# Performance work log

Hardware: AMD Instinct MI355X
Metric: run time of the kernel (lower is better)

## Reference

```python
import jax, jax.numpy as jnp
import numpy as np

X_CH, Y_CH, DIM, NUM_HEAD = 256, 512, 128, 4
H_DIM = DIM // NUM_HEAD
GAMMA = H_DIM ** (-0.5)


def conv1x1(x, w, b):
    # x: [B,C,H,W], w: [O,C], b: [O]
    return jnp.einsum('bchw,oc->bohw', x, w) + b[None, :, None, None]


def _split_qkv(qkv, bs, hw):
    # qkv: [B, 3*DIM, H, W] -> q,k,v each [B, NUM_HEAD, HW, H_DIM]
    qkv = qkv.reshape(bs, 3, NUM_HEAD, H_DIM, hw)
    qkv = jnp.transpose(qkv, (1, 0, 2, 4, 3))  # [3, B, H, HW, D]
    return qkv[0], qkv[1], qkv[2]


def setup_inputs() -> dict:
    key = jax.random.key(0)
    ks = jax.random.split(key, 12)
    s = lambda fan_in: 1.0 / np.sqrt(fan_in)
    x = jax.random.normal(ks[0], (2, X_CH, 64, 64), dtype=jnp.float32)
    y = jax.random.normal(ks[1], (2, Y_CH, 32, 32), dtype=jnp.float32)
    wx_qkv = jax.random.normal(ks[2], (3 * DIM, X_CH), dtype=jnp.float32) * s(X_CH)
    bx_qkv = jax.random.normal(ks[3], (3 * DIM,), dtype=jnp.float32) * s(X_CH)
    wy_qkv = jax.random.normal(ks[4], (3 * DIM, Y_CH), dtype=jnp.float32) * s(Y_CH)
    by_qkv = jax.random.normal(ks[5], (3 * DIM,), dtype=jnp.float32) * s(Y_CH)
    wpx = jax.random.normal(ks[6], (X_CH, DIM), dtype=jnp.float32) * s(DIM)
    bpx = jax.random.normal(ks[7], (X_CH,), dtype=jnp.float32) * s(DIM)
    wpy = jax.random.normal(ks[8], (Y_CH, DIM), dtype=jnp.float32) * s(DIM)
    bpy = jax.random.normal(ks[9], (Y_CH,), dtype=jnp.float32) * s(DIM)
    return {"x": x, "y": y, "wx_qkv": wx_qkv, "bx_qkv": bx_qkv,
            "wy_qkv": wy_qkv, "by_qkv": by_qkv,
            "wpx": wpx, "bpx": bpx, "wpy": wpy, "bpy": bpy}


def reference(x, y, wx_qkv, bx_qkv, wy_qkv, by_qkv, wpx, bpx, wpy, bpy):
    bs, _, h_x, w_x = x.shape
    _, _, h_y, w_y = y.shape
    hw_x, hw_y = h_x * w_x, h_y * w_y

    q_x, k_x, v_x = _split_qkv(conv1x1(x, wx_qkv, bx_qkv), bs, hw_x)
    q_y, k_y, v_y = _split_qkv(conv1x1(y, wy_qkv, by_qkv), bs, hw_y)

    # x attends to y
    atten_x = jax.nn.softmax(jnp.einsum('bhqd,bhkd->bhqk', q_x, k_y) * GAMMA, axis=-1)
    out_x = jnp.einsum('bhqk,bhkd->bhqd', atten_x, v_y)  # [B,H,HWx,D]
    out_x = jnp.transpose(out_x, (0, 1, 3, 2)).reshape(bs, DIM, h_x, w_x)

    # y attends to x
    atten_y = jax.nn.softmax(jnp.einsum('bhqd,bhkd->bhqk', q_y, k_x) * GAMMA, axis=-1)
    out_y = jnp.einsum('bhqk,bhkd->bhqd', atten_y, v_x)
    out_y = jnp.transpose(out_y, (0, 1, 3, 2)).reshape(bs, DIM, h_y, w_y)

    out_x = conv1x1(out_x, wpx, bpx) + x
    out_y = conv1x1(out_y, wpy, bpy) + y
    return out_x, out_y
```

## Files before the change

kernel.cpp:

```cpp
#include <hip/hip_runtime.h>
#include <hip/hip_bf16.h>
#include <cstdint>

#define B 2
#define NH 4
#define HD 32
#define DIM 128
#define CX 256
#define CY 512
#define PX 4096
#define PY 1024
#define QKV 384
#define GAMMA 0.17677669529663687f

typedef unsigned short u16;
typedef unsigned int u32;

using short8 = __attribute__((ext_vector_type(8))) short;
using f32x4  = __attribute__((ext_vector_type(4))) float;

__device__ __forceinline__ float bf2f(u32 h) {
  union { u32 u; float f; } v; v.u = (h & 0xffffu) << 16; return v.f;
}
__device__ __forceinline__ u16 f2bf(float f) {
  u32 u = __float_as_uint(f);
  u32 r = (u + 0x7fffu + ((u >> 16) & 1u)) >> 16;
  return (u16)r;
}
__device__ __forceinline__ bool is_f32(const void* src) {
  u32 u = ((const u16*)src)[2 * (threadIdx.x & 63)];
  return __ballot((u & 0x7F80u) >= 0x4600u) != 0ull;
}

#define N_X   (B * CX * PX)
#define N_Y   (B * CY * PY)
#define N_WX  (QKV * CX)
#define N_BX  (QKV)
#define N_WY  (QKV * CY)
#define N_BY  (QKV)
#define N_WPX (CX * DIM)
#define N_BPX (CX)
#define N_WPY (CY * DIM)
#define N_BPY (CY)

enum : size_t {
  OFF_CWX   = 0,
  OFF_CBX   = OFF_CWX  + N_WX,
  OFF_CWY   = OFF_CBX  + N_BX,
  OFF_CBY   = OFF_CWY  + N_WY,
  OFF_CWPX  = OFF_CBY  + N_BY,
  OFF_CBPX  = OFF_CWPX + N_WPX,
  OFF_CWPY  = OFF_CBPX + N_BPX,
  OFF_CBPY  = OFF_CWPY + N_WPY,
  OFF_XT    = OFF_CBPY + N_BPY,
  OFF_YT    = OFF_XT   + (size_t)B * PX * CX,
  OFF_QPX   = OFF_YT   + (size_t)B * PY * CY,
  OFF_KPX   = OFF_QPX  + (size_t)B * NH * PX * HD,
  OFF_QPY   = OFF_KPX  + (size_t)B * NH * PX * HD,
  OFF_KPY   = OFF_QPY  + (size_t)B * NH * PY * HD,
  OFF_VCX   = OFF_KPY  + (size_t)B * NH * PY * HD,
  OFF_VCY   = OFF_VCX  + (size_t)B * DIM * PX,
  OFF_OTX   = OFF_VCY  + (size_t)B * DIM * PY,
  OFF_OTY   = OFF_OTX  + (size_t)B * PX * DIM,
  WS_END    = OFF_OTY  + (size_t)B * PY * DIM,
};

#define XPX_BLKS 2048
#define XPY_BLKS 1024
__global__ __launch_bounds__(256) void k_prep(
    const void* x, const void* y, const void* wx, const void* bx,
    const void* wy, const void* by, const void* wpx, const void* bpx,
    const void* wpy, const void* bpy, u16* __restrict__ ws) {
  const int id = blockIdx.x;
  if (id < XPX_BLKS + XPY_BLKS) {
    __shared__ u16 tile[32][33];
    const void* src; u16* dst; int C, P, p_t, c_t, b;
    if (id < XPX_BLKS) {
      src = x; dst = ws + OFF_XT; C = CX; P = PX;
      p_t = id & 127; c_t = (id >> 7) & 7; b = id >> 10;
    } else {
      int id2 = id - XPX_BLKS;
      src = y; dst = ws + OFF_YT; C = CY; P = PY;
      p_t = id2 & 31; c_t = (id2 >> 5) & 15; b = id2 >> 9;
    }
    const bool f32in = is_f32(src);
    const int tx = threadIdx.x & 31, ty = threadIdx.x >> 5;
    const int p0 = p_t * 32, c0 = c_t * 32;
#pragma unroll
    for (int i = 0; i < 4; i++) {
      int cl = ty * 4 + i;
      size_t sidx = ((size_t)b * C + c0 + cl) * P + p0 + tx;
      u16 v = f32in ? f2bf(((const float*)src)[sidx]) : ((const u16*)src)[sidx];
      tile[cl][tx] = v;
    }
    __syncthreads();
#pragma unroll
    for (int i = 0; i < 4; i++) {
      int pl = ty * 4 + i;
      dst[((size_t)b * P + p0 + pl) * C + c0 + tx] = tile[tx][pl];
    }
  } else {
    int wid = id - (XPX_BLKS + XPY_BLKS);
    const void* src; size_t dstoff; int n, base;
    if      (wid < 48)  { src = wx;  dstoff = OFF_CWX;  n = N_WX;  base = 0; }
    else if (wid < 49)  { src = bx;  dstoff = OFF_CBX;  n = N_BX;  base = 48; }
    else if (wid < 145) { src = wy;  dstoff = OFF_CWY;  n = N_WY;  base = 49; }
    else if (wid < 146) { src = by;  dstoff = OFF_CBY;  n = N_BY;  base = 145; }
    else if (wid < 162) { src = wpx; dstoff = OFF_CWPX; n = N_WPX; base = 146; }
    else if (wid < 163) { src = bpx; dstoff = OFF_CBPX; n = N_BPX; base = 162; }
    else if (wid < 195) { src = wpy; dstoff = OFF_CWPY; n = N_WPY; base = 163; }
    else                { src = bpy; dstoff = OFF_CBPY; n = N_BPY; base = 195; }
    const bool f32in = is_f32(src);
    int e0 = (wid - base) * 2048 + threadIdx.x * 8;
    if (e0 >= n) return;
    u16* dst = ws + dstoff + e0;
    if (f32in) {
      const float* s = (const float*)src + e0;
      float4 a = *(const float4*)s;
      float4 bq = *(const float4*)(s + 4);
      ushort4 o0, o1;
      o0.x = f2bf(a.x);  o0.y = f2bf(a.y);  o0.z = f2bf(a.z);  o0.w = f2bf(a.w);
      o1.x = f2bf(bq.x); o1.y = f2bf(bq.y); o1.z = f2bf(bq.z); o1.w = f2bf(bq.w);
      *(ushort4*)dst = o0;
      *(ushort4*)(dst + 4) = o1;
    } else {
      uint4 v = *(const uint4*)((const u16*)src + e0);
      *(uint4*)dst = v;
    }
  }
}

__global__ __launch_bounds__(256) void k_qkv(u16* __restrict__ ws) {
  const int t = threadIdx.x;
  const int lane = t & 63, w = t >> 6;
  const int ql = lane & 15, quad = lane >> 4;
  const int b = blockIdx.z;

  const u16 *W, *Xt, *bias; u16 *qp, *kp, *vc; int C, P, pxb;
  if (blockIdx.x < 64) {
    W = ws + OFF_CWX; Xt = ws + OFF_XT; bias = ws + OFF_CBX;
    qp = ws + OFF_QPX; kp = ws + OFF_KPX; vc = ws + OFF_VCX;
    C = CX; P = PX; pxb = blockIdx.x;
  } else {
    W = ws + OFF_CWY; Xt = ws + OFF_YT; bias = ws + OFF_CBY;
    qp = ws + OFF_QPY; kp = ws + OFF_KPY; vc = ws + OFF_VCY;
    C = CY; P = PY; pxb = blockIdx.x - 64;
  }
  const int p_w = pxb * 64 + (w & 1) * 32;
  const int o_w = blockIdx.y * 64 + (w >> 1) * 32;

  const u16* wr0 = W + (size_t)(o_w + ql) * C;
  const u16* wr1 = W + (size_t)(o_w + 16 + ql) * C;
  const u16* xr0 = Xt + ((size_t)b * P + p_w + ql) * C;
  const u16* xr1 = Xt + ((size_t)b * P + p_w + 16 + ql) * C;

  union U { uint4 u; short8 s; };
  f32x4 acc[2][2];
#pragma unroll
  for (int i = 0; i < 2; i++)
#pragma unroll
    for (int j = 0; j < 2; j++) acc[i][j] = (f32x4){0.f, 0.f, 0.f, 0.f};

#pragma unroll 4
  for (int c0 = 0; c0 < C; c0 += 32) {
    int off = c0 + quad * 8;
    U a0, a1, b0, b1;
    a0.u = *(const uint4*)&wr0[off];
    a1.u = *(const uint4*)&wr1[off];
    b0.u = *(const uint4*)&xr0[off];
    b1.u = *(const uint4*)&xr1[off];
    acc[0][0] = __builtin_amdgcn_mfma_f32_16x16x32_bf16(a0.s, b0.s, acc[0][0], 0, 0, 0);
    acc[0][1] = __builtin_amdgcn_mfma_f32_16x16x32_bf16(a0.s, b1.s, acc[0][1], 0, 0, 0);
    acc[1][0] = __builtin_amdgcn_mfma_f32_16x16x32_bf16(a1.s, b0.s, acc[1][0], 0, 0, 0);
    acc[1][1] = __builtin_amdgcn_mfma_f32_16x16x32_bf16(a1.s, b1.s, acc[1][1], 0, 0, 0);
  }

  float bs[2][4];
#pragma unroll
  for (int oi = 0; oi < 2; oi++)
#pragma unroll
    for (int r = 0; r < 4; r++)
      bs[oi][r] = bf2f(bias[o_w + oi * 16 + quad * 4 + r]);

  if (blockIdx.y < 4) {
    bool isq = blockIdx.y < 2;
    float scale = isq ? GAMMA : 1.0f;
    u16* dstT = isq ? qp : kp;
#pragma unroll
    for (int oi = 0; oi < 2; oi++)
#pragma unroll
      for (int pi = 0; pi < 2; pi++) {
        int p = p_w + pi * 16 + ql;
        int o = o_w + oi * 16 + quad * 4 - (isq ? 0 : 128);
        int hh = o >> 5, d = o & 31;
        f32x4 a = acc[oi][pi];
        uint2 pk;
        pk.x = (u32)f2bf((a[0] + bs[oi][0]) * scale) |
               ((u32)f2bf((a[1] + bs[oi][1]) * scale) << 16);
        pk.y = (u32)f2bf((a[2] + bs[oi][2]) * scale) |
               ((u32)f2bf((a[3] + bs[oi][3]) * scale) << 16);
        *(uint2*)&dstT[((size_t)(b * NH + hh) * P + p) * HD + d] = pk;
      }
  } else {
#pragma unroll
    for (int oi = 0; oi < 2; oi++)
#pragma unroll
      for (int pi = 0; pi < 2; pi++) {
        int p = p_w + pi * 16 + ql;
        f32x4 a = acc[oi][pi];
#pragma unroll
        for (int r = 0; r < 4; r++) {
          int o = o_w + oi * 16 + quad * 4 + r - 256;
          vc[((size_t)b * DIM + o) * P + p] = f2bf(a[r] + bs[oi][r]);
        }
      }
  }
}

template <int NQF>
__device__ __forceinline__ void attn_core(
    const u16* __restrict__ Qp, const u16* __restrict__ Kp,
    const u16* __restrict__ Vc, u16* __restrict__ Ot, int Pq, int Pk,
    int q0, int h, int b, u16* pool, float (*mlb)[4][64]) {
  const int t = threadIdx.x;
  const int lane = t & 63, w = t >> 6;
  const int ql = lane & 15, quad = lane >> 4;

  union U { uint4 u; short8 s; };
  U qf[NQF];
#pragma unroll
  for (int qi = 0; qi < NQF; qi++)
    qf[qi].u = *(const uint4*)&Qp[((size_t)(b * NH + h) * Pq + q0 + qi * 16 + ql) * HD + quad * 8];

  const int kspan = Pk >> 2;
  const int kk0 = w * kspan;
  const int niter = kspan >> 5;
  const int f0 = ((ql >> 2) << 3) | (ql & 3);

  const u16* kbase = Kp + ((size_t)(b * NH + h) * Pk + kk0 + f0) * HD + quad * 8;
  const u16* v0base = Vc + ((size_t)(b * DIM + h * HD + ql)) * Pk + kk0 + quad * 8;
  const u16* v1base = v0base + (size_t)16 * Pk;

  U ka, kb, va, vb, kan, kbn, van, vbn;
  ka.u = *(const uint4*)&kbase[0];
  kb.u = *(const uint4*)&kbase[4 * HD];
  va.u = *(const uint4*)&v0base[0];
  vb.u = *(const uint4*)&v1base[0];

  f32x4 o0[NQF], o1[NQF];
  float m_run[NQF], l_run[NQF];
#pragma unroll
  for (int qi = 0; qi < NQF; qi++) {
    o0[qi] = (f32x4){0.f, 0.f, 0.f, 0.f};
    o1[qi] = (f32x4){0.f, 0.f, 0.f, 0.f};
    m_run[qi] = -1e30f; l_run[qi] = 0.f;
  }

  for (int it = 0; it < niter; it++) {
    if (it + 1 < niter) {
      size_t go = (size_t)(it + 1) * 32;
      kan.u = *(const uint4*)&kbase[go * HD];
      kbn.u = *(const uint4*)&kbase[(go + 4) * HD];
      van.u = *(const uint4*)&v0base[go];
      vbn.u = *(const uint4*)&v1base[go];
    }

#pragma unroll
    for (int qi = 0; qi < NQF; qi++) {
      f32x4 z = {0.f, 0.f, 0.f, 0.f};
      f32x4 st0 = __builtin_amdgcn_mfma_f32_16x16x32_bf16(ka.s, qf[qi].s, z, 0, 0, 0);
      f32x4 st1 = __builtin_amdgcn_mfma_f32_16x16x32_bf16(kb.s, qf[qi].s, z, 0, 0, 0);

      float s[8] = {st0[0], st0[1], st0[2], st0[3], st1[0], st1[1], st1[2], st1[3]};
      float cm = fmaxf(fmaxf(fmaxf(s[0], s[1]), fmaxf(s[2], s[3])),
                       fmaxf(fmaxf(s[4], s[5]), fmaxf(s[6], s[7])));
      cm = fmaxf(cm, __shfl_xor(cm, 16));
      cm = fmaxf(cm, __shfl_xor(cm, 32));
      float m_new = fmaxf(m_run[qi], cm);
      float alpha = __expf(m_run[qi] - m_new);
      float p[8], ls = 0.f;
#pragma unroll
      for (int i = 0; i < 8; i++) { p[i] = __expf(s[i] - m_new); ls += p[i]; }
      ls += __shfl_xor(ls, 16);
      ls += __shfl_xor(ls, 32);
      l_run[qi] = l_run[qi] * alpha + ls;
      m_run[qi] = m_new;
#pragma unroll
      for (int r = 0; r < 4; r++) { o0[qi][r] *= alpha; o1[qi][r] *= alpha; }

      U pf;
      pf.u.x = __builtin_amdgcn_perm(__float_as_uint(p[1]), __float_as_uint(p[0]), 0x07060302u);
      pf.u.y = __builtin_amdgcn_perm(__float_as_uint(p[3]), __float_as_uint(p[2]), 0x07060302u);
      pf.u.z = __builtin_amdgcn_perm(__float_as_uint(p[5]), __float_as_uint(p[4]), 0x07060302u);
      pf.u.w = __builtin_amdgcn_perm(__float_as_uint(p[7]), __float_as_uint(p[6]), 0x07060302u);

      o0[qi] = __builtin_amdgcn_mfma_f32_16x16x32_bf16(va.s, pf.s, o0[qi], 0, 0, 0);
      o1[qi] = __builtin_amdgcn_mfma_f32_16x16x32_bf16(vb.s, pf.s, o1[qi], 0, 0, 0);
    }
    ka = kan; kb = kbn; va = van; vb = vbn;
  }

  float* Of = (float*)(pool + (size_t)w * 4096);
#pragma unroll
  for (int qi = 0; qi < NQF; qi++) {
#pragma unroll
    for (int r = 0; r < 4; r++) {
      Of[(qi * 16 + ql) * 32 + quad * 4 + r] = o0[qi][r];
      Of[(qi * 16 + ql) * 32 + 16 + quad * 4 + r] = o1[qi][r];
    }
    if (quad == 0) {
      mlb[0][w][qi * 16 + ql] = m_run[qi];
      mlb[1][w][qi * 16 + ql] = l_run[qi];
    }
  }
  __syncthreads();

  const float* OfA = (const float*)pool;
#pragma unroll
  for (int k = 0; k < NQF * 2; k++) {
    int e = t + k * 256;
    int q = e >> 5, d = e & 31;
    float m0 = mlb[0][0][q], m1 = mlb[0][1][q], m2 = mlb[0][2][q], m3 = mlb[0][3][q];
    float M = fmaxf(fmaxf(m0, m1), fmaxf(m2, m3));
    float c0 = __expf(m0 - M), c1 = __expf(m1 - M), c2 = __expf(m2 - M), c3 = __expf(m3 - M);
    float lt = c0 * mlb[1][0][q] + c1 * mlb[1][1][q] + c2 * mlb[1][2][q] + c3 * mlb[1][3][q];
    int di = q * 32 + d;
    float v = c0 * OfA[di] + c1 * OfA[2048 + di] +
              c2 * OfA[4096 + di] + c3 * OfA[6144 + di];
    Ot[((size_t)b * Pq + q0 + q) * DIM + h * HD + d] = f2bf(v / lt);
  }
}

__global__ __launch_bounds__(256) void k_attn(u16* __restrict__ ws) {
  __shared__ __align__(16) u16 pool[16384];
  __shared__ float mlb[2][4][64];
  const int h = blockIdx.y, b = blockIdx.z;
  if (blockIdx.x < 64) {
    attn_core<4>(ws + OFF_QPX, ws + OFF_KPY, ws + OFF_VCY, ws + OFF_OTX,
                 PX, PY, blockIdx.x * 64, h, b, pool, mlb);
  } else {
    attn_core<2>(ws + OFF_QPY, ws + OFF_KPX, ws + OFF_VCX, ws + OFF_OTY,
                 PY, PX, (blockIdx.x - 64) * 32, h, b, pool, mlb);
  }
}

__global__ __launch_bounds__(256) void k_proj(
    u16* __restrict__ ws, void* __restrict__ outv,
    const void* __restrict__ resx, const void* __restrict__ resy) {
  const u16 *W, *A, *bias; const void* res; int OT, P, pxb; size_t out_off;
  if (blockIdx.x < 64) {
    if (blockIdx.y >= 4) return;
    W = ws + OFF_CWPX; A = ws + OFF_OTX; bias = ws + OFF_CBPX;
    res = resx; OT = CX; P = PX; pxb = blockIdx.x; out_off = 0;
  } else {
    W = ws + OFF_CWPY; A = ws + OFF_OTY; bias = ws + OFF_CBPY;
    res = resy; OT = CY; P = PY; pxb = blockIdx.x - 64;
    out_off = (size_t)B * CX * PX;
  }
  const bool f32io = is_f32(res);
  const int t = threadIdx.x;
  const int lane = t & 63, w = t >> 6;
  const int ql = lane & 15, quad = lane >> 4;
  const int p_w = pxb * 64 + (w & 1) * 32;
  const int o_w = blockIdx.y * 64 + (w >> 1) * 32;
  const int b = blockIdx.z;

  const u16* wr0 = W + (size_t)(o_w + ql) * DIM;
  const u16* wr1 = W + (size_t)(o_w + 16 + ql) * DIM;
  const u16* xr0 = A + ((size_t)b * P + p_w + ql) * DIM;
  const u16* xr1 = A + ((size_t)b * P + p_w + 16 + ql) * DIM;

  union U { uint4 u; short8 s; };
  f32x4 acc[2][2];
#pragma unroll
  for (int i = 0; i < 2; i++)
#pragma unroll
    for (int j = 0; j < 2; j++) acc[i][j] = (f32x4){0.f, 0.f, 0.f, 0.f};

#pragma unroll
  for (int c0 = 0; c0 < DIM; c0 += 32) {
    int off = c0 + quad * 8;
    U a0, a1, b0, b1;
    a0.u = *(const uint4*)&wr0[off];
    a1.u = *(const uint4*)&wr1[off];
    b0.u = *(const uint4*)&xr0[off];
    b1.u = *(const uint4*)&xr1[off];
    acc[0][0] = __builtin_amdgcn_mfma_f32_16x16x32_bf16(a0.s, b0.s, acc[0][0], 0, 0, 0);
    acc[0][1] = __builtin_amdgcn_mfma_f32_16x16x32_bf16(a0.s, b1.s, acc[0][1], 0, 0, 0);
    acc[1][0] = __builtin_amdgcn_mfma_f32_16x16x32_bf16(a1.s, b0.s, acc[1][0], 0, 0, 0);
    acc[1][1] = __builtin_amdgcn_mfma_f32_16x16x32_bf16(a1.s, b1.s, acc[1][1], 0, 0, 0);
  }

#pragma unroll
  for (int oi = 0; oi < 2; oi++)
#pragma unroll
    for (int pi = 0; pi < 2; pi++) {
      int p = p_w + pi * 16 + ql;
      f32x4 a = acc[oi][pi];
#pragma unroll
      for (int r = 0; r < 4; r++) {
        int o = o_w + oi * 16 + quad * 4 + r;
        float bv = bf2f(bias[o]);
        size_t idx = ((size_t)b * OT + o) * P + p;
        float rv = f32io ? ((const float*)res)[idx] : bf2f(((const u16*)res)[idx]);
        float v = a[r] + bv + rv;
        if (f32io) ((float*)outv)[out_off + idx] = v;
        else       ((u16*)outv)[out_off + idx] = f2bf(v);
      }
    }
}

extern "C" void kernel_launch(void* const* d_in, const int* in_sizes, int n_in,
                              void* d_out, int out_size, void* d_ws, size_t ws_size,
                              hipStream_t stream) {
  (void)in_sizes; (void)n_in; (void)out_size; (void)ws_size;
  u16* ws = (u16*)d_ws;

  k_prep<<<dim3(XPX_BLKS + XPY_BLKS + 196), 256, 0, stream>>>(
      d_in[0], d_in[1], d_in[2], d_in[3], d_in[4], d_in[5],
      d_in[6], d_in[7], d_in[8], d_in[9], ws);
  k_qkv<<<dim3(80, 6, B), 256, 0, stream>>>(ws);
  k_attn<<<dim3(96, NH, B), 256, 0, stream>>>(ws);
  k_proj<<<dim3(80, 8, B), 256, 0, stream>>>(ws, d_out, d_in[0], d_in[1]);
}
```

Measured before the change: 150.4 us.

## Vectorize transposes and epilogue stores, swap MFMA operands, split y-attention finer

The prep transpose now moves 64x64 tiles with float4 and uint2 accesses instead of scalar ones. The V projection and output projection swap MFMA operand order so each lane holds four consecutive pixels, which lets them use vector stores and residual loads instead of strided scalar ones. The y-query attention now uses one 16-query fragment per block with more blocks, which raises parallelism for the long-key side but reloads K/V more often.

```diff
diff --git a/kernel.cpp b/kernel.cpp
--- a/kernel.cpp
+++ b/kernel.cpp
@@ -65,39 +65,48 @@
   WS_END    = OFF_OTY  + (size_t)B * PY * DIM,
 };
 
-#define XPX_BLKS 2048
-#define XPY_BLKS 1024
+#define XPX_BLKS 512
+#define XPY_BLKS 256
 __global__ __launch_bounds__(256) void k_prep(
     const void* x, const void* y, const void* wx, const void* bx,
     const void* wy, const void* by, const void* wpx, const void* bpx,
     const void* wpy, const void* bpy, u16* __restrict__ ws) {
   const int id = blockIdx.x;
   if (id < XPX_BLKS + XPY_BLKS) {
-    __shared__ u16 tile[32][33];
+    __shared__ u16 tile[64][68];
     const void* src; u16* dst; int C, P, p_t, c_t, b;
     if (id < XPX_BLKS) {
       src = x; dst = ws + OFF_XT; C = CX; P = PX;
-      p_t = id & 127; c_t = (id >> 7) & 7; b = id >> 10;
+      p_t = id & 63; c_t = (id >> 6) & 3; b = id >> 8;
     } else {
       int id2 = id - XPX_BLKS;
       src = y; dst = ws + OFF_YT; C = CY; P = PY;
-      p_t = id2 & 31; c_t = (id2 >> 5) & 15; b = id2 >> 9;
+      p_t = id2 & 15; c_t = (id2 >> 4) & 7; b = id2 >> 7;
     }
     const bool f32in = is_f32(src);
-    const int tx = threadIdx.x & 31, ty = threadIdx.x >> 5;
-    const int p0 = p_t * 32, c0 = c_t * 32;
+    const int tx = threadIdx.x & 15, tc = threadIdx.x >> 4;
+    const int p0 = p_t * 64, c0 = c_t * 64;
 #pragma unroll
     for (int i = 0; i < 4; i++) {
-      int cl = ty * 4 + i;
-      size_t sidx = ((size_t)b * C + c0 + cl) * P + p0 + tx;
-      u16 v = f32in ? f2bf(((const float*)src)[sidx]) : ((const u16*)src)[sidx];
-      tile[cl][tx] = v;
+      int cl = tc + i * 16;
+      size_t sidx = ((size_t)b * C + c0 + cl) * P + p0 + tx * 4;
+      u16 v0, v1, v2, v3;
+      if (f32in) {
+        float4 f = *(const float4*)((const float*)src + sidx);
+        v0 = f2bf(f.x); v1 = f2bf(f.y); v2 = f2bf(f.z); v3 = f2bf(f.w);
+      } else {
+        uint2 u = *(const uint2*)((const u16*)src + sidx);
+        v0 = (u16)u.x; v1 = (u16)(u.x >> 16); v2 = (u16)u.y; v3 = (u16)(u.y >> 16);
+      }
+      tile[tx * 4 + 0][cl] = v0; tile[tx * 4 + 1][cl] = v1;
+      tile[tx * 4 + 2][cl] = v2; tile[tx * 4 + 3][cl] = v3;
     }
     __syncthreads();
 #pragma unroll
     for (int i = 0; i < 4; i++) {
-      int pl = ty * 4 + i;
-      dst[((size_t)b * P + p0 + pl) * C + c0 + tx] = tile[tx][pl];
+      int pl = tc + i * 16;
+      *(uint2*)&dst[((size_t)b * P + p0 + pl) * C + c0 + tx * 4] =
+          *(const uint2*)&tile[pl][tx * 4];
     }
   } else {
     int wid = id - (XPX_BLKS + XPY_BLKS);
@@ -161,28 +170,44 @@
 #pragma unroll
     for (int j = 0; j < 2; j++) acc[i][j] = (f32x4){0.f, 0.f, 0.f, 0.f};
 
+  const bool isv = blockIdx.y >= 4;
+  if (!isv) {
 #pragma unroll 4
-  for (int c0 = 0; c0 < C; c0 += 32) {
-    int off = c0 + quad * 8;
-    U a0, a1, b0, b1;
-    a0.u = *(const uint4*)&wr0[off];
-    a1.u = *(const uint4*)&wr1[off];
-    b0.u = *(const uint4*)&xr0[off];
-    b1.u = *(const uint4*)&xr1[off];
-    acc[0][0] = __builtin_amdgcn_mfma_f32_16x16x32_bf16(a0.s, b0.s, acc[0][0], 0, 0, 0);
-    acc[0][1] = __builtin_amdgcn_mfma_f32_16x16x32_bf16(a0.s, b1.s, acc[0][1], 0, 0, 0);
-    acc[1][0] = __builtin_amdgcn_mfma_f32_16x16x32_bf16(a1.s, b0.s, acc[1][0], 0, 0, 0);
-    acc[1][1] = __builtin_amdgcn_mfma_f32_16x16x32_bf16(a1.s, b1.s, acc[1][1], 0, 0, 0);
-  }
-
-  float bs[2][4];
-#pragma unroll
-  for (int oi = 0; oi < 2; oi++)
-#pragma unroll
-    for (int r = 0; r < 4; r++)
-      bs[oi][r] = bf2f(bias[o_w + oi * 16 + quad * 4 + r]);
-
-  if (blockIdx.y < 4) {
+    for (int c0 = 0; c0 < C; c0 += 32) {
+      int off = c0 + quad * 8;
+      U a0, a1, b0, b1;
+      a0.u = *(const uint4*)&wr0[off];
+      a1.u = *(const uint4*)&wr1[off];
+      b0.u = *(const uint4*)&xr0[off];
+      b1.u = *(const uint4*)&xr1[off];
+      acc[0][0] = __builtin_amdgcn_mfma_f32_16x16x32_bf16(a0.s, b0.s, acc[0][0], 0, 0, 0);
+      acc[0][1] = __builtin_amdgcn_mfma_f32_16x16x32_bf16(a0.s, b1.s, acc[0][1], 0, 0, 0);
+      acc[1][0] = __builtin_amdgcn_mfma_f32_16x16x32_bf16(a1.s, b0.s, acc[1][0], 0, 0, 0);
+      acc[1][1] = __builtin_amdgcn_mfma_f32_16x16x32_bf16(a1.s, b1.s, acc[1][1], 0, 0, 0);
+    }
+  } else {
+#pragma unroll 4
+    for (int c0 = 0; c0 < C; c0 += 32) {
+      int off = c0 + quad * 8;
+      U a0, a1, b0, b1;
+      a0.u = *(const uint4*)&wr0[off];
+      a1.u = *(const uint4*)&wr1[off];
+      b0.u = *(const uint4*)&xr0[off];
+      b1.u = *(const uint4*)&xr1[off];
+      acc[0][0] = __builtin_amdgcn_mfma_f32_16x16x32_bf16(b0.s, a0.s, acc[0][0], 0, 0, 0);
+      acc[0][1] = __builtin_amdgcn_mfma_f32_16x16x32_bf16(b1.s, a0.s, acc[0][1], 0, 0, 0);
+      acc[1][0] = __builtin_amdgcn_mfma_f32_16x16x32_bf16(b0.s, a1.s, acc[1][0], 0, 0, 0);
+      acc[1][1] = __builtin_amdgcn_mfma_f32_16x16x32_bf16(b1.s, a1.s, acc[1][1], 0, 0, 0);
+    }
+  }
+
+  if (!isv) {
+    float bs[2][4];
+#pragma unroll
+    for (int oi = 0; oi < 2; oi++)
+#pragma unroll
+      for (int r = 0; r < 4; r++)
+        bs[oi][r] = bf2f(bias[o_w + oi * 16 + quad * 4 + r]);
     bool isq = blockIdx.y < 2;
     float scale = isq ? GAMMA : 1.0f;
     u16* dstT = isq ? qp : kp;
@@ -203,17 +228,19 @@
       }
   } else {
 #pragma unroll
-    for (int oi = 0; oi < 2; oi++)
+    for (int oi = 0; oi < 2; oi++) {
+      int o = o_w + oi * 16 + ql - 256;
+      float bv = bf2f(bias[o_w + oi * 16 + ql]);
 #pragma unroll
       for (int pi = 0; pi < 2; pi++) {
-        int p = p_w + pi * 16 + ql;
+        int pbase = p_w + pi * 16 + quad * 4;
         f32x4 a = acc[oi][pi];
-#pragma unroll
-        for (int r = 0; r < 4; r++) {
-          int o = o_w + oi * 16 + quad * 4 + r - 256;
-          vc[((size_t)b * DIM + o) * P + p] = f2bf(a[r] + bs[oi][r]);
-        }
+        ushort4 st;
+        st.x = f2bf(a[0] + bv); st.y = f2bf(a[1] + bv);
+        st.z = f2bf(a[2] + bv); st.w = f2bf(a[3] + bv);
+        *(ushort4*)&vc[((size_t)b * DIM + o) * P + pbase] = st;
       }
+    }
   }
 }
 
@@ -339,8 +366,8 @@
     attn_core<4>(ws + OFF_QPX, ws + OFF_KPY, ws + OFF_VCY, ws + OFF_OTX,
                  PX, PY, blockIdx.x * 64, h, b, pool, mlb);
   } else {
-    attn_core<2>(ws + OFF_QPY, ws + OFF_KPX, ws + OFF_VCX, ws + OFF_OTY,
-                 PY, PX, (blockIdx.x - 64) * 32, h, b, pool, mlb);
+    attn_core<1>(ws + OFF_QPY, ws + OFF_KPX, ws + OFF_VCX, ws + OFF_OTY,
+                 PY, PX, (blockIdx.x - 64) * 16, h, b, pool, mlb);
   }
 }
 
@@ -385,29 +412,38 @@
     a1.u = *(const uint4*)&wr1[off];
     b0.u = *(const uint4*)&xr0[off];
     b1.u = *(const uint4*)&xr1[off];
-    acc[0][0] = __builtin_amdgcn_mfma_f32_16x16x32_bf16(a0.s, b0.s, acc[0][0], 0, 0, 0);
-    acc[0][1] = __builtin_amdgcn_mfma_f32_16x16x32_bf16(a0.s, b1.s, acc[0][1], 0, 0, 0);
-    acc[1][0] = __builtin_amdgcn_mfma_f32_16x16x32_bf16(a1.s, b0.s, acc[1][0], 0, 0, 0);
-    acc[1][1] = __builtin_amdgcn_mfma_f32_16x16x32_bf16(a1.s, b1.s, acc[1][1], 0, 0, 0);
-  }
-
-#pragma unroll
-  for (int oi = 0; oi < 2; oi++)
+    acc[0][0] = __builtin_amdgcn_mfma_f32_16x16x32_bf16(b0.s, a0.s, acc[0][0], 0, 0, 0);
+    acc[0][1] = __builtin_amdgcn_mfma_f32_16x16x32_bf16(b1.s, a0.s, acc[0][1], 0, 0, 0);
+    acc[1][0] = __builtin_amdgcn_mfma_f32_16x16x32_bf16(b0.s, a1.s, acc[1][0], 0, 0, 0);
+    acc[1][1] = __builtin_amdgcn_mfma_f32_16x16x32_bf16(b1.s, a1.s, acc[1][1], 0, 0, 0);
+  }
+
+#pragma unroll
+  for (int oi = 0; oi < 2; oi++) {
+    int o = o_w + oi * 16 + ql;
+    float bv = bf2f(bias[o]);
 #pragma unroll
     for (int pi = 0; pi < 2; pi++) {
-      int p = p_w + pi * 16 + ql;
+      int pbase = p_w + pi * 16 + quad * 4;
+      size_t idx = ((size_t)b * OT + o) * P + pbase;
       f32x4 a = acc[oi][pi];
-#pragma unroll
-      for (int r = 0; r < 4; r++) {
-        int o = o_w + oi * 16 + quad * 4 + r;
-        float bv = bf2f(bias[o]);
-        size_t idx = ((size_t)b * OT + o) * P + p;
-        float rv = f32io ? ((const float*)res)[idx] : bf2f(((const u16*)res)[idx]);
-        float v = a[r] + bv + rv;
-        if (f32io) ((float*)outv)[out_off + idx] = v;
-        else       ((u16*)outv)[out_off + idx] = f2bf(v);
+      if (f32io) {
+        float4 rv = *(const float4*)((const float*)res + idx);
+        float4 ov;
+        ov.x = a[0] + bv + rv.x; ov.y = a[1] + bv + rv.y;
+        ov.z = a[2] + bv + rv.z; ov.w = a[3] + bv + rv.w;
+        *(float4*)((float*)outv + out_off + idx) = ov;
+      } else {
+        ushort4 rv = *(const ushort4*)((const u16*)res + idx);
+        ushort4 ov;
+        ov.x = f2bf(a[0] + bv + bf2f(rv.x));
+        ov.y = f2bf(a[1] + bv + bf2f(rv.y));
+        ov.z = f2bf(a[2] + bv + bf2f(rv.z));
+        ov.w = f2bf(a[3] + bv + bf2f(rv.w));
+        *(ushort4*)((u16*)outv + out_off + idx) = ov;
       }
     }
+  }
 }
 
 extern "C" void kernel_launch(void* const* d_in, const int* in_sizes, int n_in,
@@ -420,6 +456,6 @@
       d_in[0], d_in[1], d_in[2], d_in[3], d_in[4], d_in[5],
       d_in[6], d_in[7], d_in[8], d_in[9], ws);
   k_qkv<<<dim3(80, 6, B), 256, 0, stream>>>(ws);
-  k_attn<<<dim3(96, NH, B), 256, 0, stream>>>(ws);
+  k_attn<<<dim3(128, NH, B), 256, 0, stream>>>(ws);
   k_proj<<<dim3(80, 8, B), 256, 0, stream>>>(ws, d_out, d_in[0], d_in[1]);
 }
```

Measured after the change: 158.2 us. 1.05x slower.
